# Kernel optimization log

Measured on AMD Instinct MI355X. Metric: run time of the kernel, lower is better.

Reference implementation:

```python
import jax, jax.numpy as jnp
import numpy as np
import math

T, HW, M, D, DK, H, SIGMA = 16, 1024, 256, 768, 768, 8, 0.5
HD = DK // H
VHD = D // H
EPS = 1e-6
SCALE = 1.0 / math.sqrt(HD)


def _ln(x, g):
    # LayerNorm(eps=1e-6, bias=False)
    m = x.mean(-1, keepdims=True)
    v = ((x - m) ** 2).mean(-1, keepdims=True)
    return (x - m) / jnp.sqrt(v + EPS) * g


def setup_inputs() -> dict:
    key = jax.random.key(0)
    ks = jax.random.split(key, 16)
    s = 0.02
    features = jax.random.normal(ks[0], (T, HW, D), jnp.float32)
    tracks = jax.random.uniform(ks[1], (T, M, 2), jnp.float32)
    track_pos_embeddings = jax.random.normal(ks[2], (T, M, D), jnp.float32)
    feature_pos_embeddings = jax.random.normal(ks[3], (T, HW, D), jnp.float32)
    g = jnp.linspace(0.0, 1.0, 32)
    feature_positions = jnp.stack(jnp.meshgrid(g, g, indexing='ij'), axis=-1).reshape(HW, 2)
    return {
        'features': features,
        'tracks': tracks,
        'feature_positions': feature_positions,
        'track_pos_embeddings': track_pos_embeddings,
        'feature_pos_embeddings': feature_pos_embeddings,
        # AttentionalSampling params (nn.Linear weights are [out,in])
        'Wq_s': jax.random.normal(ks[4], (DK, D)) * s,
        'Wk_s': jax.random.normal(ks[5], (DK, D)) * s,
        'Wv_s': jax.random.normal(ks[6], (D, D)) * s,
        'qg_s': jnp.ones((DK,), jnp.float32),
        'kg_s': jnp.ones((DK,), jnp.float32),
        'Wo_s': jax.random.normal(ks[7], (D, D)) * s,
        # AttentionalSplatting params
        'Wq_p': jax.random.normal(ks[8], (DK, D)) * s,
        'Wk_p': jax.random.normal(ks[9], (DK, D)) * s,
        'Wv_p': jax.random.normal(ks[10], (D, D)) * s,
        'qg_p': jnp.ones((DK,), jnp.float32),
        'kg_p': jnp.ones((DK,), jnp.float32),
        'Wout_p': jax.random.normal(ks[11], (D, D)) * s,
    }


def reference(features, tracks, feature_positions, track_pos_embeddings,
              feature_pos_embeddings, Wq_s, Wk_s, Wv_s, qg_s, kg_s, Wo_s,
              Wq_p, Wk_p, Wv_p, qg_p, kg_p, Wout_p):
    # per-frame Gaussian spatial bias from squared euclidean distances
    # d2[t,m,n] = ||tracks[t,m] - feature_positions[n]||^2  -> [T, M, HW]
    d2 = ((tracks[:, :, None, :] - feature_positions[None, None, :, :]) ** 2).sum(-1)
    bias = -d2 / (2.0 * SIGMA ** 2)  # [T, M, HW]

    # ---- Attentional Sampling: tracks query features ----
    Q = _ln(track_pos_embeddings @ Wq_s.T, qg_s)          # [T, M, DK]
    K = _ln((features + feature_pos_embeddings) @ Wk_s.T, kg_s)  # [T, HW, DK]
    V = features @ Wv_s.T                                  # [T, HW, D]
    Qh = Q.reshape(T, M, H, HD).transpose(0, 2, 1, 3)      # [T, H, M, HD]
    Kh = K.reshape(T, HW, H, HD).transpose(0, 2, 1, 3)     # [T, H, HW, HD]
    Vh = V.reshape(T, HW, H, VHD).transpose(0, 2, 1, 3)    # [T, H, HW, VHD]
    scores = jnp.einsum('thmd,thnd->thmn', Qh, Kh) * SCALE + bias[:, None]
    A = jax.nn.softmax(scores, axis=-1)
    sampled = jnp.einsum('thmn,thnd->thmd', A, Vh)
    sampled = sampled.transpose(0, 2, 1, 3).reshape(T, M, D) @ Wo_s.T  # [T, M, D]

    # ---- Attentional Splatting: features query tracks ----
    Q2 = _ln(feature_pos_embeddings @ Wq_p.T, qg_p)        # [T, HW, DK]
    K2 = _ln(track_pos_embeddings @ Wk_p.T, kg_p)          # [T, M, DK]
    V2 = sampled @ Wv_p.T                                   # [T, M, D]
    Q2h = Q2.reshape(T, HW, H, HD).transpose(0, 2, 1, 3)   # [T, H, HW, HD]
    K2h = K2.reshape(T, M, H, HD).transpose(0, 2, 1, 3)    # [T, H, M, HD]
    V2h = V2.reshape(T, M, H, VHD).transpose(0, 2, 1, 3)   # [T, H, M, VHD]
    bias_t = jnp.swapaxes(bias, 1, 2)                       # [T, HW, M] (cdist is symmetric)
    scores2 = jnp.einsum('thnd,thmd->thnm', Q2h, K2h) * SCALE + bias_t[:, None]
    A2 = jax.nn.softmax(scores2, axis=-1)
    upd = jnp.einsum('thnm,thmd->thnd', A2, V2h)
    feature_updates = upd.transpose(0, 2, 1, 3).reshape(T, HW, D) @ Wout_p.T
    return features + feature_updates
```

## Files before the change

### kernel.cpp

```cpp
#include <hip/hip_runtime.h>

#define DD 768
#define HDIM 96
#define ATT_SCALE 0.10206207261596575f

typedef float floatx4 __attribute__((ext_vector_type(4)));
typedef __bf16 bf16;
typedef bf16 bf16x8 __attribute__((ext_vector_type(8)));
typedef bf16 bf16x4 __attribute__((ext_vector_type(4)));
typedef bf16 bf16x2 __attribute__((ext_vector_type(2)));

__device__ __forceinline__ void gl2lds16(const bf16* g, bf16* l) {
  __builtin_amdgcn_global_load_lds(
      (const __attribute__((address_space(1))) void*)g,
      (__attribute__((address_space(3))) void*)l, 16, 0, 0);
}

__global__ __launch_bounds__(256) void prep(
    const float* __restrict__ features, const float* __restrict__ fpe,
    const float* __restrict__ tpe,
    const float* w0, const float* w1, const float* w2, const float* w3,
    const float* w4, const float* w5, const float* w6, const float* w7,
    bf16* __restrict__ Fb, bf16* __restrict__ Xb, bf16* __restrict__ Feb,
    bf16* __restrict__ Tb, bf16* __restrict__ Wb, bf16* __restrict__ WoT) {
  const int b = blockIdx.x;
  const int tid = threadIdx.x;
  if (b < 6144) {
    const int i = (b * 256 + tid) * 8;
    floatx4 f0 = *(const floatx4*)(features + i);
    floatx4 f1 = *(const floatx4*)(features + i + 4);
    floatx4 e0 = *(const floatx4*)(fpe + i);
    floatx4 e1 = *(const floatx4*)(fpe + i + 4);
    bf16x8 fv, xv, ev;
#pragma unroll
    for (int k = 0; k < 4; k++) {
      fv[k] = (bf16)f0[k];           fv[k + 4] = (bf16)f1[k];
      ev[k] = (bf16)e0[k];           ev[k + 4] = (bf16)e1[k];
      xv[k] = (bf16)(f0[k] + e0[k]); xv[k + 4] = (bf16)(f1[k] + e1[k]);
    }
    *(bf16x8*)(Fb + i) = fv;
    *(bf16x8*)(Xb + i) = xv;
    *(bf16x8*)(Feb + i) = ev;
  } else if (b < 7680) {
    const int i = ((b - 6144) * 256 + tid) * 8;
    floatx4 s0 = *(const floatx4*)(tpe + i);
    floatx4 s1 = *(const floatx4*)(tpe + i + 4);
    bf16x8 v;
#pragma unroll
    for (int k = 0; k < 4; k++) { v[k] = (bf16)s0[k]; v[k + 4] = (bf16)s1[k]; }
    *(bf16x8*)(Tb + i) = v;
  } else if (b < 9984) {
    const int sub = b - 7680;
    const int wi = sub / 288, xb = sub % 288;
    const float* srcs[8] = {w0, w1, w2, w3, w4, w5, w6, w7};
    const float* s = srcs[wi];
    bf16* d = Wb + (size_t)wi * 589824;
    const int i = (xb * 256 + tid) * 8;
    floatx4 s0 = *(const floatx4*)(s + i);
    floatx4 s1 = *(const floatx4*)(s + i + 4);
    bf16x8 v;
#pragma unroll
    for (int k = 0; k < 4; k++) { v[k] = (bf16)s0[k]; v[k + 4] = (bf16)s1[k]; }
    *(bf16x8*)(d + i) = v;
  } else {
    __shared__ float Ts[64][65];
    const int sub = b - 9984;
    const int X0 = (sub % 12) * 64, Y0 = (sub / 12) * 64;
    const int r = tid >> 2;
    const int c4 = (tid & 3) * 16;
    const float* src = w3 + (size_t)(Y0 + r) * DD + X0 + c4;
#pragma unroll
    for (int k = 0; k < 16; k += 4) {
      floatx4 v = *(const floatx4*)(src + k);
      Ts[r][c4 + k] = v[0]; Ts[r][c4 + k + 1] = v[1];
      Ts[r][c4 + k + 2] = v[2]; Ts[r][c4 + k + 3] = v[3];
    }
    __syncthreads();
    bf16 o[16];
#pragma unroll
    for (int k = 0; k < 16; k++) o[k] = (bf16)Ts[c4 + k][r];
    *(bf16x8*)(WoT + (size_t)(X0 + r) * DD + Y0 + c4) = *(bf16x8*)&o[0];
    *(bf16x8*)(WoT + (size_t)(X0 + r) * DD + Y0 + c4 + 8) = *(bf16x8*)&o[8];
  }
}

__device__ __forceinline__ void ln_row(bf16* x, const float* g, int lane) {
  float v[12], s = 0.f, ss = 0.f;
#pragma unroll
  for (int j = 0; j < 3; j++) {
    bf16x4 b = *(const bf16x4*)&x[j * 256 + lane * 4];
#pragma unroll
    for (int e = 0; e < 4; e++) {
      float t = (float)b[e];
      v[j * 4 + e] = t; s += t; ss += t * t;
    }
  }
#pragma unroll
  for (int o = 32; o > 0; o >>= 1) { s += __shfl_xor(s, o); ss += __shfl_xor(ss, o); }
  const float mean = s * (1.0f / DD);
  const float inv = rsqrtf(ss * (1.0f / DD) - mean * mean + 1e-6f);
#pragma unroll
  for (int j = 0; j < 3; j++) {
    floatx4 gg = *(const floatx4*)&g[j * 256 + lane * 4];
    bf16x4 o4;
#pragma unroll
    for (int e = 0; e < 4; e++) o4[e] = (bf16)((v[j * 4 + e] - mean) * inv * gg[e]);
    *(bf16x4*)&x[j * 256 + lane * 4] = o4;
  }
}

__global__ __launch_bounds__(256) void ln_all(bf16* X0, const float* g0,
                                              bf16* X1, const float* g1,
                                              bf16* X2, const float* g2,
                                              bf16* X3, const float* g3) {
  const int b = blockIdx.x;
  bf16* X; const float* g; int base;
  if (b < 4096)      { X = X0; g = g0; base = b; }
  else if (b < 8192) { X = X1; g = g1; base = b - 4096; }
  else if (b < 9216) { X = X2; g = g2; base = b - 8192; }
  else               { X = X3; g = g3; base = b - 9216; }
  const int w = threadIdx.x >> 6, lane = threadIdx.x & 63;
  ln_row(X + (size_t)(base * 4 + w) * DD, g, lane);
}

#define BAR() do { __builtin_amdgcn_sched_barrier(0); \
                   __builtin_amdgcn_s_barrier(); \
                   __builtin_amdgcn_sched_barrier(0); } while (0)
#define VMW(n) asm volatile("s_waitcnt vmcnt(" #n ")" ::: "memory")

template <int MODE>
__device__ __forceinline__ void gemm256(const bf16* __restrict__ A,
                                        const bf16* __restrict__ W,
                                        bf16* __restrict__ Cb,
                                        float* __restrict__ Cf,
                                        const float* __restrict__ addsrc,
                                        bf16* lds, int row0, int col0) {
  const int tid = threadIdx.x;
  const int lane = tid & 63;
  const int w = tid >> 6;
  const int wm = (w & 1) * 128;
  const int wn = (w >> 1) * 64;
  const int fr = lane & 15;
  const int quad = lane >> 4;
  const int f7 = fr & 7;

  const int srow = tid >> 3;
  const int sswz = ((tid & 7) ^ (srow & 7)) * 8;
  const bf16* Ag = A + (size_t)(row0 + srow) * DD + sswz;
  const bf16* Wg = W + (size_t)(col0 + srow) * DD + sswz;
  bf16* dA = lds + tid * 8;
  bf16* dB = lds + 32768 + tid * 8;

#define STGA(tau, h) do { \
    gl2lds16(Ag + (size_t)((h) * 128) * DD + (tau) * 64, \
             dA + ((tau) & 1) * 16384 + (h) * 8192); \
    gl2lds16(Ag + (size_t)((h) * 128 + 64) * DD + (tau) * 64, \
             dA + ((tau) & 1) * 16384 + (h) * 8192 + 4096); \
  } while (0)
#define STGB(tau, h) do { \
    gl2lds16(Wg + (size_t)((h) * 128) * DD + (tau) * 64, \
             dB + ((tau) & 1) * 16384 + (h) * 8192); \
    gl2lds16(Wg + (size_t)((h) * 128 + 64) * DD + (tau) * 64, \
             dB + ((tau) & 1) * 16384 + (h) * 8192 + 4096); \
  } while (0)

  const int sl0 = (quad ^ f7) * 8;
  const int sl1 = ((4 | quad) ^ f7) * 8;

#define LDA8(buf, mh) do { \
    _Pragma("unroll") for (int m = 0; m < 4; m++) { \
      const bf16* p = lds + (buf) * 16384 + (wm + (mh) * 64 + m * 16 + fr) * 64; \
      af[m][0] = *(const bf16x8*)(p + sl0); \
      af[m][1] = *(const bf16x8*)(p + sl1); } \
  } while (0)
#define LDB4(buf, nh, dst) do { \
    _Pragma("unroll") for (int n = 0; n < 2; n++) { \
      const bf16* p = lds + 32768 + (buf) * 16384 + (wn + (nh) * 32 + n * 16 + fr) * 64; \
      dst[n][0] = *(const bf16x8*)(p + sl0); \
      dst[n][1] = *(const bf16x8*)(p + sl1); } \
  } while (0)
#define MM16(mh, nbase, bb) do { \
    __builtin_amdgcn_s_setprio(1); \
    _Pragma("unroll") for (int m = 0; m < 4; m++) \
    _Pragma("unroll") for (int n = 0; n < 2; n++) { \
      acc[(mh) * 4 + m][(nbase) + n] = __builtin_amdgcn_mfma_f32_16x16x32_bf16( \
          af[m][0], bb[n][0], acc[(mh) * 4 + m][(nbase) + n], 0, 0, 0); \
      acc[(mh) * 4 + m][(nbase) + n] = __builtin_amdgcn_mfma_f32_16x16x32_bf16( \
          af[m][1], bb[n][1], acc[(mh) * 4 + m][(nbase) + n], 0, 0, 0); } \
    __builtin_amdgcn_s_setprio(0); \
  } while (0)

  floatx4 acc[8][4];

  STGB(0, 0); STGB(0, 1); STGA(0, 0); STGA(0, 1);
  STGB(1, 0); STGB(1, 1);
#pragma unroll
  for (int i = 0; i < 8; i++)
#pragma unroll
    for (int j = 0; j < 4; j++) acc[i][j] = (floatx4){0, 0, 0, 0};
  VMW(4);
  BAR();

  bf16x8 af[4][2], b0[2][2], b1[2][2];

  for (int it = 0; it < 6; ++it) {
    const int a = 2 * it;
    const bool stg = (it < 5);
    LDA8(0, 0); LDB4(0, 0, b0);
    STGA(a + 1, 0);
    BAR();
    MM16(0, 0, b0);
    BAR();
    LDB4(0, 1, b1);
    STGA(a + 1, 1);
    BAR();
    MM16(0, 2, b1);
    BAR();
    LDA8(0, 1);
    if (stg) STGB(a + 2, 0);
    BAR();
    MM16(1, 2, b1);
    BAR();
    if (stg) STGB(a + 2, 1);
    BAR();
    MM16(1, 0, b0);
    if (stg) { VMW(4); } else { VMW(0); }
    BAR();
    LDA8(1, 0); LDB4(1, 0, b0);
    if (stg) STGA(a + 2, 0);
    BAR();
    MM16(0, 0, b0);
    BAR();
    LDB4(1, 1, b1);
    if (stg) STGA(a + 2, 1);
    BAR();
    MM16(0, 2, b1);
    BAR();
    LDA8(1, 1);
    if (stg) STGB(a + 3, 0);
    BAR();
    MM16(1, 2, b1);
    BAR();
    if (stg) STGB(a + 3, 1);
    BAR();
    MM16(1, 0, b0);
    if (stg) VMW(4);
    BAR();
  }

#pragma unroll
  for (int m = 0; m < 8; m++)
#pragma unroll
    for (int n = 0; n < 4; n++)
#pragma unroll
      for (int r = 0; r < 4; r++) {
        const int row = row0 + wm + m * 16 + quad * 4 + r;
        const int col = col0 + wn + n * 16 + fr;
        const size_t idx = (size_t)row * DD + col;
        if (MODE == 0) Cb[idx] = (bf16)acc[m][n][r];
        else Cf[idx] = acc[m][n][r] + addsrc[idx];
      }
#undef STGA
#undef STGB
#undef LDA8
#undef LDB4
#undef MM16
}

__global__ __launch_bounds__(512, 2) void gemm_all(
    const bf16* Xb, const bf16* Fb, const bf16* Feb, const bf16* Tb,
    const bf16* Wb, const bf16* WoT,
    bf16* Kc, bf16* Vc, bf16* Qb2, bf16* Qc, bf16* K2, bf16* Wcr) {
  __shared__ bf16 lds[65536];
  const size_t SW = (size_t)768 * 768;
  const int z = blockIdx.z;
  if (z == 0)
    gemm256<0>(Xb, Wb + 1 * SW, Kc, nullptr, nullptr, lds,
               blockIdx.x * 256, blockIdx.y * 256);
  else if (z == 1)
    gemm256<0>(Fb, Wb + 2 * SW, Vc, nullptr, nullptr, lds,
               blockIdx.x * 256, blockIdx.y * 256);
  else if (z == 2)
    gemm256<0>(Feb, Wb + 4 * SW, Qb2, nullptr, nullptr, lds,
               blockIdx.x * 256, blockIdx.y * 256);
  else {
    const int x = blockIdx.x;
    if (x < 16)
      gemm256<0>(Tb, Wb + 0 * SW, Qc, nullptr, nullptr, lds,
                 x * 256, blockIdx.y * 256);
    else if (x < 32)
      gemm256<0>(Tb, Wb + 5 * SW, K2, nullptr, nullptr, lds,
                 (x - 16) * 256, blockIdx.y * 256);
    else if (x < 35)
      gemm256<0>(Wb + 6 * SW, WoT, Wcr, nullptr, nullptr, lds,
                 (x - 32) * 256, blockIdx.y * 256);
  }
}

__global__ __launch_bounds__(512, 2) void gemm_b(const bf16* A, const bf16* W, bf16* C) {
  __shared__ bf16 lds[65536];
  gemm256<0>(A, W, C, nullptr, nullptr, lds, blockIdx.x * 256, blockIdx.y * 256);
}

__global__ __launch_bounds__(512, 2) void gemm_final(const bf16* A, const bf16* W,
                                                     float* C, const float* addsrc) {
  __shared__ bf16 lds[65536];
  gemm256<1>(A, W, nullptr, C, addsrc, lds, blockIdx.x * 256, blockIdx.y * 256);
}

template <int SPLIT>
__global__ __launch_bounds__(512, 4) void attn512(
    const bf16* __restrict__ Qb, const bf16* __restrict__ Kb,
    const bf16* __restrict__ Vb, bf16* __restrict__ Ob,
    float* __restrict__ Ml,
    const float* __restrict__ qpos, int qpos_ts,
    const float* __restrict__ kpos, int kpos_ts,
    int nq, int nk, int npq, int nsp) {
  const int b = blockIdx.x;
  const int h = b & 7;
  const int t = (b >> 3) & 15;
  const int rest = b >> 7;
  const int qt = rest % npq;
  const int sp = rest / npq;
  const int klen = nk / nsp;
  const int k0s = sp * klen;
  const int q0 = qt * 128;
  const bf16* Q = Qb + (size_t)t * nq * DD + h * HDIM;
  const bf16* K = Kb + (size_t)t * nk * DD + h * HDIM;
  const bf16* V = Vb + (size_t)t * nk * DD + h * HDIM;
  bf16* O = Ob + (size_t)(SPLIT ? (sp * 16 + t) : t) * nq * DD + h * HDIM;
  const float* qp = qpos + (size_t)t * qpos_ts;
  const float* kp = kpos + (size_t)t * kpos_ts;

  __shared__ bf16 Ks[64 * 104];
  __shared__ bf16 Vt[96 * 72];
  __shared__ bf16 Ps[2 * 64 * 72];
  __shared__ float Kpl[512];

  const int tid = threadIdx.x;
  const int w = tid >> 6;
  const int g = w >> 2;
  const int wl = w & 3;
  const int lane = tid & 63;
  const int fr = lane & 15;
  const int quad = lane >> 4;
  const int rowb = wl * 16;
  const int qgb = q0 + g * 64;
  bf16* Pg = &Ps[g * 64 * 72];

  bf16x8 qf[3];
  {
    const bf16* qrow = Q + (size_t)(qgb + rowb + fr) * DD;
#pragma unroll
    for (int c = 0; c < 3; c++) qf[c] = *(const bf16x8*)(qrow + c * 32 + quad * 8);
  }
  float qx[4], qy[4];
#pragma unroll
  for (int r = 0; r < 4; r++) {
    int qi = qgb + rowb + quad * 4 + r;
    qx[r] = qp[qi * 2];
    qy[r] = qp[qi * 2 + 1];
  }

  float lrow[4] = {0.f, 0.f, 0.f, 0.f};
  floatx4 oacc[6];
#pragma unroll
  for (int d = 0; d < 6; d++) oacc[d] = (floatx4){0, 0, 0, 0};

  const int krA = tid >> 3, kcA = (tid & 7) * 8;
  const int krB = (tid & 255) >> 2, kcB = 64 + (tid & 3) * 8;
  const int nb = (tid & 31) * 2, db = (tid >> 5) * 6;

  Kpl[tid] = kp[(size_t)k0s * 2 + tid];

  struct VR { unsigned a, b, c; };
  bf16x8 kaA, kbA, kaB, kbB;
  VR vA0, vA1, vB0, vB1;

  auto loadreg = [&](int n0, bf16x8& ka, bf16x8& kb, VR& r0, VR& r1) {
    ka = *(const bf16x8*)(K + (size_t)(n0 + krA) * DD + kcA);
    if (tid < 256) kb = *(const bf16x8*)(K + (size_t)(n0 + krB) * DD + kcB);
    const unsigned* g0 = (const unsigned*)(V + (size_t)(n0 + nb) * DD + db);
    const unsigned* g1 = (const unsigned*)(V + (size_t)(n0 + nb + 1) * DD + db);
    r0.a = g0[0]; r0.b = g0[1]; r0.c = g0[2];
    r1.a = g1[0]; r1.b = g1[1]; r1.c = g1[2];
  };
  auto writelds = [&](const bf16x8& ka, const bf16x8& kb, const VR& r0, const VR& r1) {
    *(bf16x8*)&Ks[krA * 104 + kcA] = ka;
    if (tid < 256) *(bf16x8*)&Ks[krB * 104 + kcB] = kb;
    bf16 t0[6], t1[6];
    *(unsigned*)&t0[0] = r0.a; *(unsigned*)&t0[2] = r0.b; *(unsigned*)&t0[4] = r0.c;
    *(unsigned*)&t1[0] = r1.a; *(unsigned*)&t1[2] = r1.b; *(unsigned*)&t1[4] = r1.c;
#pragma unroll
    for (int dd = 0; dd < 6; dd++) {
      bf16x2 v2 = {t0[dd], t1[dd]};
      *(bf16x2*)&Vt[(db + dd) * 72 + nb] = v2;
    }
  };
  auto compute = [&](int rel) {
    floatx4 s4[4];
#pragma unroll
    for (int j = 0; j < 4; j++) {
      floatx4 sa = {0, 0, 0, 0};
#pragma unroll
      for (int c = 0; c < 3; c++) {
        bf16x8 kf = *(const bf16x8*)&Ks[(j * 16 + fr) * 104 + c * 32 + quad * 8];
        sa = __builtin_amdgcn_mfma_f32_16x16x32_bf16(qf[c], kf, sa, 0, 0, 0);
      }
      s4[j] = sa;
    }
    float kxx[4], kyy[4];
#pragma unroll
    for (int j = 0; j < 4; j++) {
      int ki = (rel + j * 16 + fr) * 2;
      kxx[j] = Kpl[ki];
      kyy[j] = Kpl[ki + 1];
    }
#pragma unroll
    for (int j = 0; j < 4; j++)
#pragma unroll
      for (int r = 0; r < 4; r++) {
        float dx = qx[r] - kxx[j], dy = qy[r] - kyy[j];
        float sv = s4[j][r] * ATT_SCALE - 2.0f * (dx * dx + dy * dy);
        float pv = __expf(sv);
        lrow[r] += pv;
        Pg[(rowb + quad * 4 + r) * 72 + j * 16 + fr] = (bf16)pv;
      }
    bf16x8 pf0 = *(const bf16x8*)&Pg[(rowb + fr) * 72 + quad * 8];
    bf16x8 pf1 = *(const bf16x8*)&Pg[(rowb + fr) * 72 + 32 + quad * 8];
#pragma unroll
    for (int d = 0; d < 6; d++) {
      bf16x8 v0 = *(const bf16x8*)&Vt[(d * 16 + fr) * 72 + quad * 8];
      bf16x8 v1 = *(const bf16x8*)&Vt[(d * 16 + fr) * 72 + 32 + quad * 8];
      oacc[d] = __builtin_amdgcn_mfma_f32_16x16x32_bf16(pf0, v0, oacc[d], 0, 0, 0);
      oacc[d] = __builtin_amdgcn_mfma_f32_16x16x32_bf16(pf1, v1, oacc[d], 0, 0, 0);
    }
  };

  const int NT = klen >> 6;
  loadreg(k0s, kaA, kbA, vA0, vA1);
  for (int n = 0; n < NT; n += 2) {
    __syncthreads();
    writelds(kaA, kbA, vA0, vA1);
    if (n + 1 < NT) loadreg(k0s + (n + 1) * 64, kaB, kbB, vB0, vB1);
    __syncthreads();
    compute(n * 64);
    if (n + 1 >= NT) break;
    __syncthreads();
    writelds(kaB, kbB, vB0, vB1);
    if (n + 2 < NT) loadreg(k0s + (n + 2) * 64, kaA, kbA, vA0, vA1);
    __syncthreads();
    compute((n + 1) * 64);
  }

#pragma unroll
  for (int r = 0; r < 4; r++)
#pragma unroll
    for (int o = 1; o < 16; o <<= 1) lrow[r] += __shfl_xor(lrow[r], o);

#pragma unroll
  for (int r = 0; r < 4; r++) {
    int row = qgb + rowb + quad * 4 + r;
    if (SPLIT) {
#pragma unroll
      for (int d = 0; d < 6; d++)
        O[(size_t)row * DD + d * 16 + fr] = (bf16)oacc[d][r];
      if (fr == 0)
        Ml[((size_t)(sp * 16 + t) * 8 + h) * nq + row] = lrow[r];
    } else {
      float inv = 1.0f / lrow[r];
#pragma unroll
      for (int d = 0; d < 6; d++)
        O[(size_t)row * DD + d * 16 + fr] = (bf16)(oacc[d][r] * inv);
    }
  }
}

__global__ __launch_bounds__(256) void combine4(const bf16* __restrict__ Op,
                                                const float* __restrict__ Ml,
                                                bf16* __restrict__ Out) {
  const int row = blockIdx.x;
  const int t = row >> 8;
  const int q = row & 255;
#pragma unroll
  for (int e = 0; e < 3; e++) {
    int dim = threadIdx.x + e * 256;
    int hh = dim / 96;
    float osum = 0.f, lsum = 0.f;
#pragma unroll
    for (int s = 0; s < 4; s++) {
      lsum += Ml[((size_t)(s * 16 + t) * 8 + hh) * 256 + q];
      osum += (float)Op[((size_t)(s * 16 + t) * 256 + q) * DD + dim];
    }
    Out[(size_t)row * DD + dim] = (bf16)(osum / lsum);
  }
}

extern "C" void kernel_launch(void* const* d_in, const int* in_sizes, int n_in,
                              void* d_out, int out_size, void* d_ws, size_t ws_size,
                              hipStream_t stream) {
  const float* features = (const float*)d_in[0];
  const float* tracks   = (const float*)d_in[1];
  const float* fpos     = (const float*)d_in[2];
  const float* tpe      = (const float*)d_in[3];
  const float* fpe      = (const float*)d_in[4];
  const float* Wq_s     = (const float*)d_in[5];
  const float* Wk_s     = (const float*)d_in[6];
  const float* Wv_s     = (const float*)d_in[7];
  const float* qg_s     = (const float*)d_in[8];
  const float* kg_s     = (const float*)d_in[9];
  const float* Wo_s     = (const float*)d_in[10];
  const float* Wq_p     = (const float*)d_in[11];
  const float* Wk_p     = (const float*)d_in[12];
  const float* Wv_p     = (const float*)d_in[13];
  const float* qg_p     = (const float*)d_in[14];
  const float* kg_p     = (const float*)d_in[15];
  const float* Wout_p   = (const float*)d_in[16];
  float* out = (float*)d_out;

  const size_t SB = (size_t)16 * 1024 * 768;
  const size_t SS = (size_t)16 * 256 * 768;
  const size_t SW = (size_t)768 * 768;
  bf16* p = (bf16*)d_ws;
  bf16* Fb  = p; p += SB;
  bf16* Xb  = p; p += SB;
  bf16* Feb = p; p += SB;
  bf16* Kc  = p; p += SB;
  bf16* Vc  = p; p += SB;
  bf16* Qb2 = p; p += SB;
  bf16* Tb  = p; p += SS;
  bf16* Qc  = p; p += SS;
  bf16* K2  = p; p += SS;
  bf16* Sh  = p; p += SS;
  bf16* Op  = p; p += 4 * SS;
  bf16* Wb  = p; p += 8 * SW;
  bf16* WoT = p; p += SW;
  bf16* Wcr = p; p += SW;
  float* Ml = (float*)p;
  bf16* V2 = Qc; bf16* U = Fb;

  dim3 blk(256);

  prep<<<10128, blk, 0, stream>>>(features, fpe, tpe,
                                  Wq_s, Wk_s, Wv_s, Wo_s, Wq_p, Wk_p, Wv_p, Wout_p,
                                  Fb, Xb, Feb, Tb, Wb, WoT);
  gemm_all<<<dim3(64, 3, 4), dim3(512), 0, stream>>>(Xb, Fb, Feb, Tb, Wb, WoT,
                                                     Kc, Vc, Qb2, Qc, K2, Wcr);
  ln_all<<<10240, blk, 0, stream>>>(Kc, kg_s, Qb2, qg_p, Qc, qg_s, K2, kg_p);
  attn512<1><<<1024, dim3(512), 0, stream>>>(Qc, Kc, Vc, Op, Ml,
                                             tracks, 512, fpos, 0, 256, 1024, 2, 4);
  combine4<<<4096, blk, 0, stream>>>(Op, Ml, Sh);
  gemm_b<<<dim3(16, 3), dim3(512), 0, stream>>>(Sh, Wcr, V2);
  attn512<0><<<1024, dim3(512), 0, stream>>>(Qb2, K2, V2, U, nullptr,
                                             fpos, 0, tracks, 512, 1024, 256, 8, 1);
  gemm_final<<<dim3(64, 3), dim3(512), 0, stream>>>(U, Wb + 7 * SW, out, features);
}
```

Measured before the change: 436.5 us.

## Stage GEMM epilogue through LDS for vector stores; load V synchronously in attention

The GEMM epilogue now writes accumulators to a per-wave LDS scratch tile and reads them back row-contiguous, so each lane emits 16-byte bf16x8 or float4 stores (and float4 residual loads) instead of scattered scalar stores. Separately, the attention loop stops prefetching V into registers a tile ahead; V is loaded right before the LDS transpose, which cuts register pressure but exposes that load latency. The loop also drops the odd-NT break, which assumes an even tile count.

```diff
diff --git a/kernel.cpp b/kernel.cpp
--- a/kernel.cpp
+++ b/kernel.cpp
@@ -127,6 +127,8 @@
                    __builtin_amdgcn_s_barrier(); \
                    __builtin_amdgcn_sched_barrier(0); } while (0)
 #define VMW(n) asm volatile("s_waitcnt vmcnt(" #n ")" ::: "memory")
+#define LGKM0() do { asm volatile("s_waitcnt lgkmcnt(0)" ::: "memory"); \
+                     __builtin_amdgcn_sched_barrier(0); } while (0)
 
 template <int MODE>
 __device__ __forceinline__ void gemm256(const bf16* __restrict__ A,
@@ -248,18 +250,42 @@
     BAR();
   }
 
-#pragma unroll
-  for (int m = 0; m < 8; m++)
+  float* sc = (float*)lds + (size_t)w * (16 * 68);
+  const int er = lane >> 2;
+  const int ec = lane & 3;
+#pragma unroll
+  for (int m = 0; m < 8; m++) {
 #pragma unroll
     for (int n = 0; n < 4; n++)
 #pragma unroll
-      for (int r = 0; r < 4; r++) {
-        const int row = row0 + wm + m * 16 + quad * 4 + r;
-        const int col = col0 + wn + n * 16 + fr;
-        const size_t idx = (size_t)row * DD + col;
-        if (MODE == 0) Cb[idx] = (bf16)acc[m][n][r];
-        else Cf[idx] = acc[m][n][r] + addsrc[idx];
+      for (int r = 0; r < 4; r++)
+        sc[(quad * 4 + r) * 68 + n * 16 + fr] = acc[m][n][r];
+    LGKM0();
+    floatx4 rv[4];
+#pragma unroll
+    for (int c = 0; c < 4; c++) rv[c] = *(const floatx4*)&sc[er * 68 + ec * 16 + c * 4];
+    LGKM0();
+    const int grow = row0 + wm + m * 16 + er;
+    const int gcol = col0 + wn + ec * 16;
+    if (MODE == 0) {
+      bf16x8 o0, o1;
+#pragma unroll
+      for (int e = 0; e < 8; e++) {
+        o0[e] = (bf16)rv[e >> 2][e & 3];
+        o1[e] = (bf16)rv[2 + (e >> 2)][e & 3];
       }
+      *(bf16x8*)(Cb + (size_t)grow * DD + gcol) = o0;
+      *(bf16x8*)(Cb + (size_t)grow * DD + gcol + 8) = o1;
+    } else {
+      const float* as = addsrc + (size_t)grow * DD + gcol;
+      float* cp = Cf + (size_t)grow * DD + gcol;
+#pragma unroll
+      for (int c = 0; c < 4; c++) {
+        floatx4 av = *(const floatx4*)(as + c * 4);
+        *(floatx4*)(cp + c * 4) = rv[c] + av;
+      }
+    }
+  }
 #undef STGA
 #undef STGB
 #undef LDA8
@@ -373,24 +399,22 @@
 
   Kpl[tid] = kp[(size_t)k0s * 2 + tid];
 
-  struct VR { unsigned a, b, c; };
   bf16x8 kaA, kbA, kaB, kbB;
-  VR vA0, vA1, vB0, vB1;
-
-  auto loadreg = [&](int n0, bf16x8& ka, bf16x8& kb, VR& r0, VR& r1) {
+
+  auto loadK = [&](int n0, bf16x8& ka, bf16x8& kb) {
     ka = *(const bf16x8*)(K + (size_t)(n0 + krA) * DD + kcA);
     if (tid < 256) kb = *(const bf16x8*)(K + (size_t)(n0 + krB) * DD + kcB);
-    const unsigned* g0 = (const unsigned*)(V + (size_t)(n0 + nb) * DD + db);
-    const unsigned* g1 = (const unsigned*)(V + (size_t)(n0 + nb + 1) * DD + db);
-    r0.a = g0[0]; r0.b = g0[1]; r0.c = g0[2];
-    r1.a = g1[0]; r1.b = g1[1]; r1.c = g1[2];
   };
-  auto writelds = [&](const bf16x8& ka, const bf16x8& kb, const VR& r0, const VR& r1) {
+  auto stageKV = [&](const bf16x8& ka, const bf16x8& kb, int n0) {
     *(bf16x8*)&Ks[krA * 104 + kcA] = ka;
     if (tid < 256) *(bf16x8*)&Ks[krB * 104 + kcB] = kb;
     bf16 t0[6], t1[6];
-    *(unsigned*)&t0[0] = r0.a; *(unsigned*)&t0[2] = r0.b; *(unsigned*)&t0[4] = r0.c;
-    *(unsigned*)&t1[0] = r1.a; *(unsigned*)&t1[2] = r1.b; *(unsigned*)&t1[4] = r1.c;
+    const unsigned* g0 = (const unsigned*)(V + (size_t)(n0 + nb) * DD + db);
+    const unsigned* g1 = (const unsigned*)(V + (size_t)(n0 + nb + 1) * DD + db);
+    unsigned u0 = g0[0], u1 = g0[1], u2 = g0[2];
+    unsigned x0 = g1[0], x1 = g1[1], x2 = g1[2];
+    *(unsigned*)&t0[0] = u0; *(unsigned*)&t0[2] = u1; *(unsigned*)&t0[4] = u2;
+    *(unsigned*)&t1[0] = x0; *(unsigned*)&t1[2] = x1; *(unsigned*)&t1[4] = x2;
 #pragma unroll
     for (int dd = 0; dd < 6; dd++) {
       bf16x2 v2 = {t0[dd], t1[dd]};
@@ -438,17 +462,16 @@
   };
 
   const int NT = klen >> 6;
-  loadreg(k0s, kaA, kbA, vA0, vA1);
+  loadK(k0s, kaA, kbA);
   for (int n = 0; n < NT; n += 2) {
     __syncthreads();
-    writelds(kaA, kbA, vA0, vA1);
-    if (n + 1 < NT) loadreg(k0s + (n + 1) * 64, kaB, kbB, vB0, vB1);
+    stageKV(kaA, kbA, k0s + n * 64);
+    if (n + 1 < NT) loadK(k0s + (n + 1) * 64, kaB, kbB);
     __syncthreads();
     compute(n * 64);
-    if (n + 1 >= NT) break;
     __syncthreads();
-    writelds(kaB, kbB, vB0, vB1);
-    if (n + 2 < NT) loadreg(k0s + (n + 2) * 64, kaA, kbA, vA0, vA1);
+    stageKV(kaB, kbB, k0s + (n + 1) * 64);
+    if (n + 2 < NT) loadK(k0s + (n + 2) * 64, kaA, kbA);
     __syncthreads();
     compute((n + 1) * 64);
   }
```

Result: slower. 448.2 us (+2.7%).
